# Optimization experiments

Measured on AMD Instinct MI355X. Metric: run time of the kernel, lower is better.

## Reference

```python
import jax, jax.numpy as jnp
import numpy as np

B, H, S, D = 2, 16, 2048, 64


def setup_inputs() -> dict:
    key = jax.random.key(0)
    kq, kk, kv, km = jax.random.split(key, 4)
    q = jax.random.normal(kq, (B, H, S, D), dtype=jnp.float32)
    k = jax.random.normal(kk, (B, H, S, D), dtype=jnp.float32)
    v = jax.random.normal(kv, (B, H, S, D), dtype=jnp.float32)
    # True = attend, False = masked out (padding)
    attention_mask = jax.random.randint(km, (B, S), 0, 2).astype(jnp.bool_)
    return {"q": q, "k": k, "v": v, "attention_mask": attention_mask}


def reference(q, k, v, attention_mask):
    scale = q.shape[-1] ** -0.5
    # sim: [B, H, S, S]
    sim = jnp.einsum("bhid,bhjd->bhij", q, k) * scale
    neg = jnp.finfo(sim.dtype).min
    # mask [B, S] -> [B, 1, 1, S]; keep where mask is True
    sim = jnp.where(attention_mask[:, None, None, :], sim, neg)
    attn = jax.nn.softmax(sim, axis=-1)
    out = jnp.einsum("bhij,bhjd->bhid", attn, v)
    return out
```

## Files before the change

### kernel.cpp

```cpp
#include <hip/hip_runtime.h>
#include <hip/hip_fp16.h>

namespace {
constexpr int kB = 2, kH = 16, kS = 2048, kD = 64, kBH = kB * kH;
constexpr int BQ = 128, BKV = 64;
constexpr int NQT = kS / BQ;

typedef _Float16 f16x8 __attribute__((ext_vector_type(8)));
typedef _Float16 f16x4 __attribute__((ext_vector_type(4)));
typedef __fp16 fp16x2 __attribute__((ext_vector_type(2)));
typedef float f32x16 __attribute__((ext_vector_type(16)));
typedef float f32x4 __attribute__((ext_vector_type(4)));
typedef unsigned int u32;

constexpr float kQScale = 0.125f * 1.4426950408889634f;

__device__ __forceinline__ int paddr(int row, int col) {
  const int prow = row >> 1;
  return prow * 128 + ((((row & 1) << 6) | col) ^ ((prow & 15) << 3));
}

__device__ __forceinline__ u32 pkrtz(float a, float b) {
  union { fp16x2 h; u32 u; } c;
  c.h = __builtin_amdgcn_cvt_pkrtz(a, b);
  return c.u;
}

__global__ __launch_bounds__(256) void scan_kernel(const int* __restrict__ M,
                                                   int* __restrict__ Idx,
                                                   int* __restrict__ NTarr,
                                                   int* __restrict__ Nvarr) {
  const int b = blockIdx.x;
  const int tid = threadIdx.x;
  __shared__ int part[256];
  __shared__ int nvs;
  int m[8], sum = 0;
#pragma unroll
  for (int i = 0; i < 8; ++i) {
    m[i] = M[b * kS + tid * 8 + i];
    sum += m[i] ? 1 : 0;
  }
  part[tid] = sum;
  __syncthreads();
  for (int off = 1; off < 256; off <<= 1) {
    int v = (tid >= off) ? part[tid - off] : 0;
    __syncthreads();
    part[tid] += v;
    __syncthreads();
  }
  int run = part[tid] - sum;
#pragma unroll
  for (int i = 0; i < 8; ++i)
    if (m[i]) Idx[b * kS + run++] = tid * 8 + i;
  if (tid == 255) nvs = part[255];
  __syncthreads();
  const int Nv = nvs;
  int NT = (Nv + 63) >> 6;
  if (NT == 0) NT = 1;
  const int pad = NT * 64;
  for (int j = Nv + tid; j < pad; j += 256) Idx[b * kS + j] = 0;
  if (tid == 0) { NTarr[b] = NT; Nvarr[b] = Nv; }
}

__global__ __launch_bounds__(256) void gather_kv_kernel(
    const float* __restrict__ K, const float* __restrict__ V,
    const int* __restrict__ Idx, const int* __restrict__ NTarr,
    _Float16* __restrict__ Kc, _Float16* __restrict__ Vtc) {
  __shared__ _Float16 Vl[64 * 68];
  __shared__ int ridx[64];
  const int tid = threadIdx.x;
  const int bh = blockIdx.x >> 5;
  const int jt = blockIdx.x & 31;
  const int b = bh >> 4;
  if (jt >= NTarr[b]) return;
  if (tid < 64) ridx[tid] = Idx[b * kS + jt * 64 + tid];
  __syncthreads();

  const float* kbase = K + (size_t)bh * kS * kD;
  _Float16* kout = Kc + ((size_t)bh * kS + jt * 64) * kD;
#pragma unroll
  for (int it = 0; it < 2; ++it) {
    const int e = tid + 256 * it;
    const int row = e >> 3, d0 = (e & 7) * 8;
    const float* p = kbase + (size_t)ridx[row] * kD + d0;
    float4 x = *(const float4*)p;
    float4 y = *(const float4*)(p + 4);
    f16x8 o;
    o[0] = (_Float16)x.x; o[1] = (_Float16)x.y; o[2] = (_Float16)x.z; o[3] = (_Float16)x.w;
    o[4] = (_Float16)y.x; o[5] = (_Float16)y.y; o[6] = (_Float16)y.z; o[7] = (_Float16)y.w;
    *(f16x8*)(kout + (size_t)row * kD + d0) = o;
  }

  const float* vb = V + (size_t)bh * kS * kD;
#pragma unroll
  for (int i = 0; i < 4; ++i) {
    int off = (tid + 256 * i) * 4;
    int r = off >> 6, c = off & 63;
    float4 x = *(const float4*)(vb + (size_t)ridx[r] * kD + c);
    Vl[(c + 0) * 68 + r] = (_Float16)x.x;
    Vl[(c + 1) * 68 + r] = (_Float16)x.y;
    Vl[(c + 2) * 68 + r] = (_Float16)x.z;
    Vl[(c + 3) * 68 + r] = (_Float16)x.w;
  }
  __syncthreads();
  const int d = tid >> 2, c0 = (tid & 3) * 16;
  _Float16* op = Vtc + ((size_t)bh * kD + d) * kS + jt * 64 + c0;
#pragma unroll
  for (int j = 0; j < 4; ++j)
    *(f16x4*)(op + 4 * j) = *(const f16x4*)(Vl + d * 68 + c0 + 4 * j);
}

__global__ __launch_bounds__(256, 2) void fattn_c(
    const _Float16* __restrict__ Kc, const _Float16* __restrict__ Vtc,
    const float* __restrict__ Q, const int* __restrict__ NTarr,
    const int* __restrict__ Nvarr, float* __restrict__ O) {
  __shared__ __align__(16) char smem[32768];
  _Float16* Kl = (_Float16*)smem;
  _Float16* Vl = (_Float16*)(smem + 16384);
  float* Os = (float*)smem;

  const int tid = threadIdx.x;
  const int lane = tid & 63;
  const int w = tid >> 6;
  const int q = lane & 31;
  const int h = lane >> 5;

  const int bid = blockIdx.x;
  const int cpx = gridDim.x >> 3;
  const int sbid = (bid & 7) * cpx + (bid >> 3);
  const int bh = sbid >> 4;
  const int qt = sbid & 15;
  const int q0 = qt * BQ;
  const int b = bh >> 4;
  const int NT = NTarr[b];
  const int Nv = Nvarr[b];

  f16x8 qf[4];
  {
    const float* qp = Q + ((size_t)bh * kS + q0 + w * 32 + q) * kD;
#pragma unroll
    for (int dc = 0; dc < 4; ++dc) {
      const float* p = qp + dc * 16 + h * 8;
      float4 x = *(const float4*)p;
      float4 y = *(const float4*)(p + 4);
      f16x8 a;
      a[0] = (_Float16)(x.x * kQScale); a[1] = (_Float16)(x.y * kQScale);
      a[2] = (_Float16)(x.z * kQScale); a[3] = (_Float16)(x.w * kQScale);
      a[4] = (_Float16)(y.x * kQScale); a[5] = (_Float16)(y.y * kQScale);
      a[6] = (_Float16)(y.z * kQScale); a[7] = (_Float16)(y.w * kQScale);
      qf[dc] = a;
    }
  }

  f32x16 oa[2];
#pragma unroll
  for (int i = 0; i < 16; ++i) { oa[0][i] = 0.f; oa[1][i] = 0.f; }
  f32x16 kZero;
#pragma unroll
  for (int i = 0; i < 16; ++i) kZero[i] = 0.f;
  float m_run = -30.f, l_run = 0.f;

  const _Float16* kb = Kc + (size_t)bh * kS * kD;
  const _Float16* vb = Vtc + (size_t)bh * kD * kS;

  const int sr = tid >> 2, sc = (tid & 3) * 16;
  const int a0 = paddr(sr, sc), a1 = paddr(sr, sc + 8);

  {
    f16x8 k0 = *(const f16x8*)(kb + (size_t)sr * kD + sc);
    f16x8 k1 = *(const f16x8*)(kb + (size_t)sr * kD + sc + 8);
    f16x8 v0 = *(const f16x8*)(vb + (size_t)sr * kS + sc);
    f16x8 v1 = *(const f16x8*)(vb + (size_t)sr * kS + sc + 8);
    *(f16x8*)(Kl + a0) = k0; *(f16x8*)(Kl + a1) = k1;
    *(f16x8*)(Vl + a0) = v0; *(f16x8*)(Vl + a1) = v1;
  }
  __syncthreads();

  int cur = 0;
  for (int t = 0; t < NT; ++t) {
    const int t0 = t * BKV;
    const bool pf = (t + 1 < NT);
    f16x8 nk0, nk1, nv0, nv1;
    if (pf) {
      const int n0 = t0 + BKV;
      nk0 = *(const f16x8*)(kb + (size_t)(n0 + sr) * kD + sc);
      nk1 = *(const f16x8*)(kb + (size_t)(n0 + sr) * kD + sc + 8);
      nv0 = *(const f16x8*)(vb + (size_t)sr * kS + n0 + sc);
      nv1 = *(const f16x8*)(vb + (size_t)sr * kS + n0 + sc + 8);
    }

    const _Float16* kd = Kl + cur * 4096;
    const _Float16* vd = Vl + cur * 4096;

    f32x16 s[2];
    __builtin_amdgcn_s_setprio(1);
#pragma unroll
    for (int mt = 0; mt < 2; ++mt) {
      f32x16 z = kZero;
#pragma unroll
      for (int dc = 0; dc < 4; ++dc) {
        f16x8 kf = *(const f16x8*)(kd + paddr(mt * 32 + q, dc * 16 + h * 8));
        z = __builtin_amdgcn_mfma_f32_32x32x16_f16(kf, qf[dc], z, 0, 0, 0);
      }
      s[mt] = z;
    }
    __builtin_amdgcn_s_setprio(0);

    if (t == NT - 1) {
      const int kbase = t0 + 4 * h;
#pragma unroll
      for (int mt = 0; mt < 2; ++mt)
#pragma unroll
        for (int r = 0; r < 16; ++r) {
          const int key = kbase + mt * 32 + 8 * (r >> 2) + (r & 3);
          if (key >= Nv) s[mt][r] = -1e30f;
        }
    }

    float tm[16];
#pragma unroll
    for (int i = 0; i < 16; ++i) tm[i] = fmaxf(s[0][i], s[1][i]);
#pragma unroll
    for (int st = 8; st > 0; st >>= 1)
#pragma unroll
      for (int i = 0; i < st; ++i) tm[i] = fmaxf(tm[i], tm[i + st]);
    const float mx = fmaxf(tm[0], __shfl_xor(tm[0], 32));

    if (__any(mx > m_run + 8.f)) {
      const float mnew = fmaxf(m_run, mx);
      const float corr = __builtin_amdgcn_exp2f(m_run - mnew);
      m_run = mnew;
      l_run *= corr;
#pragma unroll
      for (int mt = 0; mt < 2; ++mt)
#pragma unroll
        for (int r = 0; r < 16; ++r) oa[mt][r] *= corr;
    }
    const float negm = -m_run;

#pragma unroll
    for (int mt = 0; mt < 2; ++mt)
#pragma unroll
      for (int r = 0; r < 16; ++r)
        s[mt][r] = __builtin_amdgcn_exp2f(s[mt][r] + negm);
    float tsum[16];
#pragma unroll
    for (int i = 0; i < 16; ++i) tsum[i] = s[0][i] + s[1][i];
#pragma unroll
    for (int st = 8; st > 0; st >>= 1)
#pragma unroll
      for (int i = 0; i < st; ++i) tsum[i] += tsum[i + st];
    l_run += tsum[0] + __shfl_xor(tsum[0], 32);

    u32 pkA[2][4], pkB[2][4];
#pragma unroll
    for (int mt = 0; mt < 2; ++mt)
#pragma unroll
      for (int g = 0; g < 4; ++g) {
        pkA[mt][g] = pkrtz(s[mt][4 * g + 0], s[mt][4 * g + 1]);
        pkB[mt][g] = pkrtz(s[mt][4 * g + 2], s[mt][4 * g + 3]);
      }

    __builtin_amdgcn_s_setprio(1);
#pragma unroll
    for (int kk = 0; kk < 4; ++kk) {
      const int e = kk & 1, mt = kk >> 1;
      u32 crossA = __shfl_xor(h ? pkA[mt][2 * e] : pkA[mt][2 * e + 1], 32);
      u32 crossB = __shfl_xor(h ? pkB[mt][2 * e] : pkB[mt][2 * e + 1], 32);
      union { u32 u[4]; f16x8 v; } pb;
      pb.u[0] = h ? crossA : pkA[mt][2 * e];
      pb.u[1] = h ? crossB : pkB[mt][2 * e];
      pb.u[2] = h ? pkA[mt][2 * e + 1] : crossA;
      pb.u[3] = h ? pkB[mt][2 * e + 1] : crossB;
#pragma unroll
      for (int md = 0; md < 2; ++md) {
        f16x8 vf = *(const f16x8*)(vd + paddr(md * 32 + q, kk * 16 + h * 8));
        oa[md] = __builtin_amdgcn_mfma_f32_32x32x16_f16(vf, pb.v, oa[md], 0, 0, 0);
      }
    }
    __builtin_amdgcn_s_setprio(0);

    if (pf) {
      _Float16* kd2 = Kl + (cur ^ 1) * 4096;
      _Float16* vd2 = Vl + (cur ^ 1) * 4096;
      *(f16x8*)(kd2 + a0) = nk0; *(f16x8*)(kd2 + a1) = nk1;
      *(f16x8*)(vd2 + a0) = nv0; *(f16x8*)(vd2 + a1) = nv1;
    }
    __syncthreads();
    cur ^= 1;
  }

  const float inv = 1.f / l_run;
#pragma unroll
  for (int ph = 0; ph < 2; ++ph) {
    __syncthreads();
    if ((w >> 1) == ph) {
#pragma unroll
      for (int mt = 0; mt < 2; ++mt)
#pragma unroll
        for (int r = 0; r < 16; ++r) {
          int d = mt * 32 + (r & 3) + 8 * (r >> 2) + 4 * h;
          Os[((w & 1) * 32 + q) * 68 + d] = oa[mt][r] * inv;
        }
    }
    __syncthreads();
    {
      const int row = tid >> 2, cb = (tid & 3) * 16;
      float* op = O + ((size_t)bh * kS + q0 + ph * 64 + row) * kD + cb;
      const float* sp = Os + row * 68 + cb;
#pragma unroll
      for (int j = 0; j < 4; ++j) *(float4*)(op + 4 * j) = *(const float4*)(sp + 4 * j);
    }
  }
}

__device__ __forceinline__ int swz(int row, int colh) {
  return row * 64 + (colh ^ ((row & 7) << 3));
}

__global__ __launch_bounds__(256, 4) void fattn_fallback(
    const float* __restrict__ Q, const float* __restrict__ K,
    const float* __restrict__ V, const int* __restrict__ M,
    float* __restrict__ O) {
  __shared__ __align__(16) _Float16 Kl[64 * 64];
  __shared__ __align__(16) _Float16 Vtl[64 * 64];
  __shared__ __align__(16) _Float16 Pl[64 * 64];
  __shared__ float mbl[64];

  const int tid = threadIdx.x;
  const int lane = tid & 63;
  const int w = tid >> 6;
  const int lr = lane & 15;
  const int hg = lane >> 4;
  const int NQT1 = kS / 64;
  const int bh = blockIdx.x / NQT1;
  const int qt = blockIdx.x % NQT1;
  const int b = bh / kH;
  const int q0 = qt * 64;

  f16x8 aq[2];
  {
    const int row = q0 + w * 16 + lr;
    const float* qp = Q + ((size_t)bh * kS + row) * kD;
#pragma unroll
    for (int kf = 0; kf < 2; ++kf) {
      const float* p = qp + kf * 32 + hg * 8;
      float4 x = *(const float4*)(p);
      float4 y = *(const float4*)(p + 4);
      f16x8 a;
      a[0] = (_Float16)(x.x * 0.125f); a[1] = (_Float16)(x.y * 0.125f);
      a[2] = (_Float16)(x.z * 0.125f); a[3] = (_Float16)(x.w * 0.125f);
      a[4] = (_Float16)(y.x * 0.125f); a[5] = (_Float16)(y.y * 0.125f);
      a[6] = (_Float16)(y.z * 0.125f); a[7] = (_Float16)(y.w * 0.125f);
      aq[kf] = a;
    }
  }

  f32x4 oacc[4];
#pragma unroll
  for (int c = 0; c < 4; ++c) { oacc[c][0]=0.f; oacc[c][1]=0.f; oacc[c][2]=0.f; oacc[c][3]=0.f; }
  float m_run[4], l_run[4];
#pragma unroll
  for (int r = 0; r < 4; ++r) { m_run[r] = -1e30f; l_run[r] = 0.f; }

  const float* kb = K + (size_t)bh * kS * kD;
  const float* vb = V + (size_t)bh * kS * kD;
  const int* mbp = M + b * kS;

  for (int t0 = 0; t0 < kS; t0 += 64) {
    __syncthreads();
#pragma unroll
    for (int i = 0; i < 4; ++i) {
      const int off = (tid + 256 * i) * 4;
      const int row = off >> 6;
      const int col = off & 63;
      float4 kx = *(const float4*)(kb + (size_t)(t0 + row) * kD + col);
      f16x4 hk;
      hk[0] = (_Float16)kx.x; hk[1] = (_Float16)kx.y;
      hk[2] = (_Float16)kx.z; hk[3] = (_Float16)kx.w;
      *(f16x4*)(Kl + swz(row, col)) = hk;
      float4 vx = *(const float4*)(vb + (size_t)(t0 + row) * kD + col);
      Vtl[swz(col + 0, row)] = (_Float16)vx.x;
      Vtl[swz(col + 1, row)] = (_Float16)vx.y;
      Vtl[swz(col + 2, row)] = (_Float16)vx.z;
      Vtl[swz(col + 3, row)] = (_Float16)vx.w;
    }
    if (tid < 64) mbl[tid] = mbp[t0 + tid] ? 0.f : -1e30f;
    __syncthreads();

    f32x4 s[4];
#pragma unroll
    for (int c = 0; c < 4; ++c) {
      f32x4 z; z[0]=0.f; z[1]=0.f; z[2]=0.f; z[3]=0.f;
#pragma unroll
      for (int kf = 0; kf < 2; ++kf) {
        f16x8 bk = *(const f16x8*)(Kl + swz(c * 16 + lr, kf * 32 + hg * 8));
        z = __builtin_amdgcn_mfma_f32_16x16x32_f16(aq[kf], bk, z, 0, 0, 0);
      }
      const float mval = mbl[c * 16 + lr];
#pragma unroll
      for (int r = 0; r < 4; ++r) z[r] += mval;
      s[c] = z;
    }

    float tmax[4];
#pragma unroll
    for (int r = 0; r < 4; ++r)
      tmax[r] = fmaxf(fmaxf(s[0][r], s[1][r]), fmaxf(s[2][r], s[3][r]));
#pragma unroll
    for (int off = 1; off < 16; off <<= 1)
#pragma unroll
      for (int r = 0; r < 4; ++r) tmax[r] = fmaxf(tmax[r], __shfl_xor(tmax[r], off));

    float mnew[4], corr[4], tsum[4];
#pragma unroll
    for (int r = 0; r < 4; ++r) {
      mnew[r] = fmaxf(m_run[r], tmax[r]);
      corr[r] = __expf(m_run[r] - mnew[r]);
      m_run[r] = mnew[r];
      tsum[r] = 0.f;
    }
#pragma unroll
    for (int c = 0; c < 4; ++c)
#pragma unroll
      for (int r = 0; r < 4; ++r) {
        const float p = __expf(s[c][r] - mnew[r]);
        tsum[r] += p;
        Pl[swz(w * 16 + hg * 4 + r, c * 16 + lr)] = (_Float16)p;
      }
#pragma unroll
    for (int off = 1; off < 16; off <<= 1)
#pragma unroll
      for (int r = 0; r < 4; ++r) tsum[r] += __shfl_xor(tsum[r], off);
#pragma unroll
    for (int r = 0; r < 4; ++r) l_run[r] = l_run[r] * corr[r] + tsum[r];
#pragma unroll
    for (int c = 0; c < 4; ++c)
#pragma unroll
      for (int r = 0; r < 4; ++r) oacc[c][r] *= corr[r];

#pragma unroll
    for (int kf = 0; kf < 2; ++kf) {
      f16x8 pa = *(const f16x8*)(Pl + swz(w * 16 + lr, kf * 32 + hg * 8));
#pragma unroll
      for (int cd = 0; cd < 4; ++cd) {
        f16x8 vbf = *(const f16x8*)(Vtl + swz(cd * 16 + lr, kf * 32 + hg * 8));
        oacc[cd] = __builtin_amdgcn_mfma_f32_16x16x32_f16(pa, vbf, oacc[cd], 0, 0, 0);
      }
    }
  }

#pragma unroll
  for (int r = 0; r < 4; ++r) {
    const float inv = 1.f / l_run[r];
    const int row = q0 + w * 16 + hg * 4 + r;
    float* op = O + ((size_t)bh * kS + row) * kD;
#pragma unroll
    for (int cd = 0; cd < 4; ++cd) op[cd * 16 + lr] = oacc[cd][r] * inv;
  }
}
}

extern "C" void kernel_launch(void* const* d_in, const int* in_sizes, int n_in,
                              void* d_out, int out_size, void* d_ws, size_t ws_size,
                              hipStream_t stream) {
  (void)in_sizes; (void)n_in; (void)out_size;
  const float* q = (const float*)d_in[0];
  const float* k = (const float*)d_in[1];
  const float* v = (const float*)d_in[2];
  const int* m = (const int*)d_in[3];
  float* o = (float*)d_out;

  const size_t elems = (size_t)kBH * kS * kD;
  const size_t need = 2 * elems * sizeof(_Float16)
                    + (size_t)kB * kS * sizeof(int)
                    + 512;

  if (ws_size >= need) {
    _Float16* Kc = (_Float16*)d_ws;
    _Float16* Vtc = Kc + elems;
    int* Idx = (int*)(Vtc + elems);
    int* NTarr = Idx + (size_t)kB * kS;
    int* Nvarr = NTarr + 64;
    hipLaunchKernelGGL(scan_kernel, dim3(kB), dim3(256), 0, stream, m, Idx, NTarr, Nvarr);
    hipLaunchKernelGGL(gather_kv_kernel, dim3(kBH * (kS / 64)), dim3(256), 0, stream,
                       k, v, Idx, NTarr, Kc, Vtc);
    hipLaunchKernelGGL(fattn_c, dim3(kBH * NQT), dim3(256), 0, stream,
                       Kc, Vtc, q, NTarr, Nvarr, o);
  } else {
    hipLaunchKernelGGL(fattn_fallback, dim3(kBH * (kS / 64)), dim3(256), 0, stream,
                       q, k, v, m, o);
  }
}
```

Baseline: 52.35 us.

## Split KV range across two warp groups per block and merge softmax partials

```diff
diff --git a/kernel.cpp b/kernel.cpp
--- a/kernel.cpp
+++ b/kernel.cpp
@@ -10,7 +10,6 @@
 typedef _Float16 f16x4 __attribute__((ext_vector_type(4)));
 typedef __fp16 fp16x2 __attribute__((ext_vector_type(2)));
 typedef float f32x16 __attribute__((ext_vector_type(16)));
-typedef float f32x4 __attribute__((ext_vector_type(4)));
 typedef unsigned int u32;
 
 constexpr float kQScale = 0.125f * 1.4426950408889634f;
@@ -57,6 +56,7 @@
   const int Nv = nvs;
   int NT = (Nv + 63) >> 6;
   if (NT == 0) NT = 1;
+  NT += (NT & 1);
   const int pad = NT * 64;
   for (int j = Nv + tid; j < pad; j += 256) Idx[b * kS + j] = 0;
   if (tid == 0) { NTarr[b] = NT; Nvarr[b] = Nv; }
@@ -110,20 +110,19 @@
     *(f16x4*)(op + 4 * j) = *(const f16x4*)(Vl + d * 68 + c0 + 4 * j);
 }
 
-__global__ __launch_bounds__(256, 2) void fattn_c(
+__global__ __launch_bounds__(512, 4) void fattn8(
     const _Float16* __restrict__ Kc, const _Float16* __restrict__ Vtc,
     const float* __restrict__ Q, const int* __restrict__ NTarr,
     const int* __restrict__ Nvarr, float* __restrict__ O) {
-  __shared__ __align__(16) char smem[32768];
-  _Float16* Kl = (_Float16*)smem;
-  _Float16* Vl = (_Float16*)(smem + 16384);
-  float* Os = (float*)smem;
+  __shared__ __align__(16) char smem[66560];
 
   const int tid = threadIdx.x;
   const int lane = tid & 63;
-  const int w = tid >> 6;
   const int q = lane & 31;
   const int h = lane >> 5;
+  const int half = tid >> 8;
+  const int ptid = tid & 255;
+  const int hw = ptid >> 6;
 
   const int bid = blockIdx.x;
   const int cpx = gridDim.x >> 3;
@@ -134,10 +133,14 @@
   const int b = bh >> 4;
   const int NT = NTarr[b];
   const int Nv = Nvarr[b];
+  const int NTh = NT >> 1;
+  const int g0 = half * NTh;
+
+  _Float16* Kl = (_Float16*)(smem + half * 16384);
 
   f16x8 qf[4];
   {
-    const float* qp = Q + ((size_t)bh * kS + q0 + w * 32 + q) * kD;
+    const float* qp = Q + ((size_t)bh * kS + q0 + hw * 32 + q) * kD;
 #pragma unroll
     for (int dc = 0; dc < 4; ++dc) {
       const float* p = qp + dc * 16 + h * 8;
@@ -155,48 +158,48 @@
   f32x16 oa[2];
 #pragma unroll
   for (int i = 0; i < 16; ++i) { oa[0][i] = 0.f; oa[1][i] = 0.f; }
-  f32x16 kZero;
-#pragma unroll
-  for (int i = 0; i < 16; ++i) kZero[i] = 0.f;
   float m_run = -30.f, l_run = 0.f;
 
   const _Float16* kb = Kc + (size_t)bh * kS * kD;
   const _Float16* vb = Vtc + (size_t)bh * kD * kS;
-
-  const int sr = tid >> 2, sc = (tid & 3) * 16;
+  const _Float16* vrow0 = vb + (size_t)q * kS + h * 8;
+  const _Float16* vrow1 = vb + (size_t)(q + 32) * kS + h * 8;
+
+  const int sr = ptid >> 2, sc = (ptid & 3) * 16;
   const int a0 = paddr(sr, sc), a1 = paddr(sr, sc + 8);
 
-  {
-    f16x8 k0 = *(const f16x8*)(kb + (size_t)sr * kD + sc);
-    f16x8 k1 = *(const f16x8*)(kb + (size_t)sr * kD + sc + 8);
-    f16x8 v0 = *(const f16x8*)(vb + (size_t)sr * kS + sc);
-    f16x8 v1 = *(const f16x8*)(vb + (size_t)sr * kS + sc + 8);
-    *(f16x8*)(Kl + a0) = k0; *(f16x8*)(Kl + a1) = k1;
-    *(f16x8*)(Vl + a0) = v0; *(f16x8*)(Vl + a1) = v1;
-  }
+  f16x8 nk0, nk1, vr[8];
+
+  nk0 = *(const f16x8*)(kb + (size_t)(g0 * 64 + sr) * kD + sc);
+  nk1 = *(const f16x8*)(kb + (size_t)(g0 * 64 + sr) * kD + sc + 8);
+  *(f16x8*)(Kl + a0) = nk0;
+  *(f16x8*)(Kl + a1) = nk1;
   __syncthreads();
 
   int cur = 0;
-  for (int t = 0; t < NT; ++t) {
-    const int t0 = t * BKV;
-    const bool pf = (t + 1 < NT);
-    f16x8 nk0, nk1, nv0, nv1;
+  for (int i = 0; i < NTh; ++i) {
+    const int g = g0 + i;
+#pragma unroll
+    for (int kk = 0; kk < 4; ++kk) {
+      vr[kk] = *(const f16x8*)(vrow0 + g * 64 + kk * 16);
+      vr[4 + kk] = *(const f16x8*)(vrow1 + g * 64 + kk * 16);
+    }
+    const bool pf = (i + 1 < NTh);
     if (pf) {
-      const int n0 = t0 + BKV;
+      const int n0 = (g + 1) * 64;
       nk0 = *(const f16x8*)(kb + (size_t)(n0 + sr) * kD + sc);
       nk1 = *(const f16x8*)(kb + (size_t)(n0 + sr) * kD + sc + 8);
-      nv0 = *(const f16x8*)(vb + (size_t)sr * kS + n0 + sc);
-      nv1 = *(const f16x8*)(vb + (size_t)sr * kS + n0 + sc + 8);
     }
 
     const _Float16* kd = Kl + cur * 4096;
-    const _Float16* vd = Vl + cur * 4096;
 
     f32x16 s[2];
     __builtin_amdgcn_s_setprio(1);
 #pragma unroll
     for (int mt = 0; mt < 2; ++mt) {
-      f32x16 z = kZero;
+      f32x16 z;
+#pragma unroll
+      for (int i2 = 0; i2 < 16; ++i2) z[i2] = 0.f;
 #pragma unroll
       for (int dc = 0; dc < 4; ++dc) {
         f16x8 kf = *(const f16x8*)(kd + paddr(mt * 32 + q, dc * 16 + h * 8));
@@ -206,8 +209,8 @@
     }
     __builtin_amdgcn_s_setprio(0);
 
-    if (t == NT - 1) {
-      const int kbase = t0 + 4 * h;
+    if ((g + 1) * 64 > Nv) {
+      const int kbase = g * 64 + 4 * h;
 #pragma unroll
       for (int mt = 0; mt < 2; ++mt)
 #pragma unroll
@@ -219,11 +222,11 @@
 
     float tm[16];
 #pragma unroll
-    for (int i = 0; i < 16; ++i) tm[i] = fmaxf(s[0][i], s[1][i]);
+    for (int i2 = 0; i2 < 16; ++i2) tm[i2] = fmaxf(s[0][i2], s[1][i2]);
 #pragma unroll
     for (int st = 8; st > 0; st >>= 1)
 #pragma unroll
-      for (int i = 0; i < st; ++i) tm[i] = fmaxf(tm[i], tm[i + st]);
+      for (int i2 = 0; i2 < st; ++i2) tm[i2] = fmaxf(tm[i2], tm[i2 + st]);
     const float mx = fmaxf(tm[0], __shfl_xor(tm[0], 32));
 
     if (__any(mx > m_run + 8.f)) {
@@ -245,20 +248,20 @@
         s[mt][r] = __builtin_amdgcn_exp2f(s[mt][r] + negm);
     float tsum[16];
 #pragma unroll
-    for (int i = 0; i < 16; ++i) tsum[i] = s[0][i] + s[1][i];
+    for (int i2 = 0; i2 < 16; ++i2) tsum[i2] = s[0][i2] + s[1][i2];
 #pragma unroll
     for (int st = 8; st > 0; st >>= 1)
 #pragma unroll
-      for (int i = 0; i < st; ++i) tsum[i] += tsum[i + st];
+      for (int i2 = 0; i2 < st; ++i2) tsum[i2] += tsum[i2 + st];
     l_run += tsum[0] + __shfl_xor(tsum[0], 32);
 
     u32 pkA[2][4], pkB[2][4];
 #pragma unroll
     for (int mt = 0; mt < 2; ++mt)
 #pragma unroll
-      for (int g = 0; g < 4; ++g) {
-        pkA[mt][g] = pkrtz(s[mt][4 * g + 0], s[mt][4 * g + 1]);
-        pkB[mt][g] = pkrtz(s[mt][4 * g + 2], s[mt][4 * g + 3]);
+      for (int g2 = 0; g2 < 4; ++g2) {
+        pkA[mt][g2] = pkrtz(s[mt][4 * g2 + 0], s[mt][4 * g2 + 1]);
+        pkB[mt][g2] = pkrtz(s[mt][4 * g2 + 2], s[mt][4 * g2 + 3]);
       }
 
     __builtin_amdgcn_s_setprio(1);
@@ -273,43 +276,66 @@
       pb.u[2] = h ? pkA[mt][2 * e + 1] : crossA;
       pb.u[3] = h ? pkB[mt][2 * e + 1] : crossB;
 #pragma unroll
-      for (int md = 0; md < 2; ++md) {
-        f16x8 vf = *(const f16x8*)(vd + paddr(md * 32 + q, kk * 16 + h * 8));
-        oa[md] = __builtin_amdgcn_mfma_f32_32x32x16_f16(vf, pb.v, oa[md], 0, 0, 0);
-      }
+      for (int md = 0; md < 2; ++md)
+        oa[md] = __builtin_amdgcn_mfma_f32_32x32x16_f16(vr[md * 4 + kk], pb.v,
+                                                        oa[md], 0, 0, 0);
     }
     __builtin_amdgcn_s_setprio(0);
 
     if (pf) {
       _Float16* kd2 = Kl + (cur ^ 1) * 4096;
-      _Float16* vd2 = Vl + (cur ^ 1) * 4096;
-      *(f16x8*)(kd2 + a0) = nk0; *(f16x8*)(kd2 + a1) = nk1;
-      *(f16x8*)(vd2 + a0) = nv0; *(f16x8*)(vd2 + a1) = nv1;
+      *(f16x8*)(kd2 + a0) = nk0;
+      *(f16x8*)(kd2 + a1) = nk1;
     }
     __syncthreads();
     cur ^= 1;
   }
 
-  const float inv = 1.f / l_run;
+  float* O1 = (float*)(smem + 32768);
+  float* ml1 = (float*)(smem + 65536);
+  if (half == 1) {
+#pragma unroll
+    for (int mt = 0; mt < 2; ++mt)
+#pragma unroll
+      for (int r = 0; r < 16; ++r) {
+        const int d = mt * 32 + (r & 3) + 8 * (r >> 2) + 4 * h;
+        O1[(hw * 32 + q) * 64 + d] = oa[mt][r];
+      }
+    if (h == 0)
+      ((float2*)ml1)[hw * 32 + q] = make_float2(m_run, l_run);
+  }
+  __syncthreads();
+  float w0 = 0.f, w1 = 0.f;
+  if (half == 0) {
+    const float2 m1 = ((const float2*)ml1)[hw * 32 + q];
+    const float mm = fmaxf(m_run, m1.x);
+    w0 = __builtin_amdgcn_exp2f(m_run - mm);
+    w1 = __builtin_amdgcn_exp2f(m1.x - mm);
+    const float inv = 1.f / (l_run * w0 + m1.y * w1);
+    w0 *= inv;
+    w1 *= inv;
+  }
+  float* Os = (float*)smem;
 #pragma unroll
   for (int ph = 0; ph < 2; ++ph) {
     __syncthreads();
-    if ((w >> 1) == ph) {
+    if (half == 0 && (hw >> 1) == ph) {
 #pragma unroll
       for (int mt = 0; mt < 2; ++mt)
 #pragma unroll
         for (int r = 0; r < 16; ++r) {
-          int d = mt * 32 + (r & 3) + 8 * (r >> 2) + 4 * h;
-          Os[((w & 1) * 32 + q) * 68 + d] = oa[mt][r] * inv;
+          const int d = mt * 32 + (r & 3) + 8 * (r >> 2) + 4 * h;
+          const int gqr = hw * 32 + q;
+          Os[((hw & 1) * 32 + q) * 68 + d] = oa[mt][r] * w0 + O1[gqr * 64 + d] * w1;
         }
     }
     __syncthreads();
     {
-      const int row = tid >> 2, cb = (tid & 3) * 16;
-      float* op = O + ((size_t)bh * kS + q0 + ph * 64 + row) * kD + cb;
-      const float* sp = Os + row * 68 + cb;
-#pragma unroll
-      for (int j = 0; j < 4; ++j) *(float4*)(op + 4 * j) = *(const float4*)(sp + 4 * j);
+      const int row = tid >> 3, c0 = (tid & 7) * 8;
+      float* op = O + ((size_t)bh * kS + q0 + ph * 64 + row) * kD + c0;
+      const float* sp = Os + row * 68 + c0;
+      *(float4*)op = *(const float4*)sp;
+      *(float4*)(op + 4) = *(const float4*)(sp + 4);
     }
   }
 }
@@ -356,6 +382,7 @@
     }
   }
 
+  typedef float f32x4 __attribute__((ext_vector_type(4)));
   f32x4 oacc[4];
 #pragma unroll
   for (int c = 0; c < 4; ++c) { oacc[c][0]=0.f; oacc[c][1]=0.f; oacc[c][2]=0.f; oacc[c][3]=0.f; }
@@ -485,7 +512,7 @@
     hipLaunchKernelGGL(scan_kernel, dim3(kB), dim3(256), 0, stream, m, Idx, NTarr, Nvarr);
     hipLaunchKernelGGL(gather_kv_kernel, dim3(kBH * (kS / 64)), dim3(256), 0, stream,
                        k, v, Idx, NTarr, Kc, Vtc);
-    hipLaunchKernelGGL(fattn_c, dim3(kBH * NQT), dim3(256), 0, stream,
+    hipLaunchKernelGGL(fattn8, dim3(kBH * NQT), dim3(512), 0, stream,
                        Kc, Vtc, q, NTarr, Nvarr, o);
   } else {
     hipLaunchKernelGGL(fattn_fallback, dim3(kBH * (kS / 64)), dim3(256), 0, stream,
```

Measured after the change: 103.5 us. +97.8%, slower.

## Process two KV tiles per iteration with 64KB double-buffered shared memory

Applied to the files above, without the earlier changes.

```diff
diff --git a/kernel.cpp b/kernel.cpp
--- a/kernel.cpp
+++ b/kernel.cpp
@@ -3,14 +3,13 @@
 
 namespace {
 constexpr int kB = 2, kH = 16, kS = 2048, kD = 64, kBH = kB * kH;
-constexpr int BQ = 128, BKV = 64;
+constexpr int BQ = 128;
 constexpr int NQT = kS / BQ;
 
 typedef _Float16 f16x8 __attribute__((ext_vector_type(8)));
 typedef _Float16 f16x4 __attribute__((ext_vector_type(4)));
 typedef __fp16 fp16x2 __attribute__((ext_vector_type(2)));
 typedef float f32x16 __attribute__((ext_vector_type(16)));
-typedef float f32x4 __attribute__((ext_vector_type(4)));
 typedef unsigned int u32;
 
 constexpr float kQScale = 0.125f * 1.4426950408889634f;
@@ -57,6 +56,7 @@
   const int Nv = nvs;
   int NT = (Nv + 63) >> 6;
   if (NT == 0) NT = 1;
+  NT += (NT & 1);
   const int pad = NT * 64;
   for (int j = Nv + tid; j < pad; j += 256) Idx[b * kS + j] = 0;
   if (tid == 0) { NTarr[b] = NT; Nvarr[b] = Nv; }
@@ -114,9 +114,9 @@
     const _Float16* __restrict__ Kc, const _Float16* __restrict__ Vtc,
     const float* __restrict__ Q, const int* __restrict__ NTarr,
     const int* __restrict__ Nvarr, float* __restrict__ O) {
-  __shared__ __align__(16) char smem[32768];
+  __shared__ __align__(16) char smem[65536];
   _Float16* Kl = (_Float16*)smem;
-  _Float16* Vl = (_Float16*)(smem + 16384);
+  _Float16* Vl = (_Float16*)(smem + 32768);
   float* Os = (float*)smem;
 
   const int tid = threadIdx.x;
@@ -134,6 +134,7 @@
   const int b = bh >> 4;
   const int NT = NTarr[b];
   const int Nv = Nvarr[b];
+  const int NP = NT >> 1;
 
   f16x8 qf[4];
   {
@@ -155,9 +156,6 @@
   f32x16 oa[2];
 #pragma unroll
   for (int i = 0; i < 16; ++i) { oa[0][i] = 0.f; oa[1][i] = 0.f; }
-  f32x16 kZero;
-#pragma unroll
-  for (int i = 0; i < 16; ++i) kZero[i] = 0.f;
   float m_run = -30.f, l_run = 0.f;
 
   const _Float16* kb = Kc + (size_t)bh * kS * kD;
@@ -166,64 +164,78 @@
   const int sr = tid >> 2, sc = (tid & 3) * 16;
   const int a0 = paddr(sr, sc), a1 = paddr(sr, sc + 8);
 
-  {
-    f16x8 k0 = *(const f16x8*)(kb + (size_t)sr * kD + sc);
-    f16x8 k1 = *(const f16x8*)(kb + (size_t)sr * kD + sc + 8);
-    f16x8 v0 = *(const f16x8*)(vb + (size_t)sr * kS + sc);
-    f16x8 v1 = *(const f16x8*)(vb + (size_t)sr * kS + sc + 8);
-    *(f16x8*)(Kl + a0) = k0; *(f16x8*)(Kl + a1) = k1;
-    *(f16x8*)(Vl + a0) = v0; *(f16x8*)(Vl + a1) = v1;
-  }
+  f16x8 nk0, nk1, nv0, nv1;
+  auto loadT = [&](int g) {
+    const _Float16* kp = kb + (size_t)(g * 64 + sr) * kD + sc;
+    const _Float16* vp = vb + (size_t)sr * kS + g * 64 + sc;
+    nk0 = *(const f16x8*)(kp);
+    nk1 = *(const f16x8*)(kp + 8);
+    nv0 = *(const f16x8*)(vp);
+    nv1 = *(const f16x8*)(vp + 8);
+  };
+  auto writeT = [&](int buf, int sub) {
+    _Float16* kd = Kl + buf * 8192 + sub * 4096;
+    _Float16* vd = Vl + buf * 8192 + sub * 4096;
+    *(f16x8*)(kd + a0) = nk0; *(f16x8*)(kd + a1) = nk1;
+    *(f16x8*)(vd + a0) = nv0; *(f16x8*)(vd + a1) = nv1;
+  };
+
+  loadT(0); writeT(0, 0);
+  loadT(1); writeT(0, 1);
   __syncthreads();
 
   int cur = 0;
-  for (int t = 0; t < NT; ++t) {
-    const int t0 = t * BKV;
-    const bool pf = (t + 1 < NT);
-    f16x8 nk0, nk1, nv0, nv1;
-    if (pf) {
-      const int n0 = t0 + BKV;
-      nk0 = *(const f16x8*)(kb + (size_t)(n0 + sr) * kD + sc);
-      nk1 = *(const f16x8*)(kb + (size_t)(n0 + sr) * kD + sc + 8);
-      nv0 = *(const f16x8*)(vb + (size_t)sr * kS + n0 + sc);
-      nv1 = *(const f16x8*)(vb + (size_t)sr * kS + n0 + sc + 8);
-    }
-
-    const _Float16* kd = Kl + cur * 4096;
-    const _Float16* vd = Vl + cur * 4096;
-
-    f32x16 s[2];
+  for (int i = 0; i < NP; ++i) {
+    const bool pf = (i + 1 < NP);
+    if (pf) loadT(2 * i + 2);
+
+    const _Float16* kd = Kl + cur * 8192;
+    const _Float16* vd = Vl + cur * 8192;
+
+    f32x16 s[4];
     __builtin_amdgcn_s_setprio(1);
 #pragma unroll
-    for (int mt = 0; mt < 2; ++mt) {
-      f32x16 z = kZero;
-#pragma unroll
-      for (int dc = 0; dc < 4; ++dc) {
-        f16x8 kf = *(const f16x8*)(kd + paddr(mt * 32 + q, dc * 16 + h * 8));
-        z = __builtin_amdgcn_mfma_f32_32x32x16_f16(kf, qf[dc], z, 0, 0, 0);
-      }
-      s[mt] = z;
-    }
+    for (int sub = 0; sub < 2; ++sub)
+#pragma unroll
+      for (int mt = 0; mt < 2; ++mt) {
+        f32x16 z;
+#pragma unroll
+        for (int i2 = 0; i2 < 16; ++i2) z[i2] = 0.f;
+#pragma unroll
+        for (int dc = 0; dc < 4; ++dc) {
+          f16x8 kf = *(const f16x8*)(kd + sub * 4096 +
+                                     paddr(mt * 32 + q, dc * 16 + h * 8));
+          z = __builtin_amdgcn_mfma_f32_32x32x16_f16(kf, qf[dc], z, 0, 0, 0);
+        }
+        s[sub * 2 + mt] = z;
+      }
     __builtin_amdgcn_s_setprio(0);
 
-    if (t == NT - 1) {
-      const int kbase = t0 + 4 * h;
-#pragma unroll
-      for (int mt = 0; mt < 2; ++mt)
-#pragma unroll
-        for (int r = 0; r < 16; ++r) {
-          const int key = kbase + mt * 32 + 8 * (r >> 2) + (r & 3);
-          if (key >= Nv) s[mt][r] = -1e30f;
-        }
+    if (pf) writeT(cur ^ 1, 0);
+    if (pf) loadT(2 * i + 3);
+
+    if ((i + 1) * 128 > Nv) {
+#pragma unroll
+      for (int sub = 0; sub < 2; ++sub) {
+        const int kbase = i * 128 + sub * 64 + 4 * h;
+#pragma unroll
+        for (int mt = 0; mt < 2; ++mt)
+#pragma unroll
+          for (int r = 0; r < 16; ++r) {
+            const int key = kbase + mt * 32 + 8 * (r >> 2) + (r & 3);
+            if (key >= Nv) s[sub * 2 + mt][r] = -1e30f;
+          }
+      }
     }
 
     float tm[16];
 #pragma unroll
-    for (int i = 0; i < 16; ++i) tm[i] = fmaxf(s[0][i], s[1][i]);
+    for (int i2 = 0; i2 < 16; ++i2)
+      tm[i2] = fmaxf(fmaxf(s[0][i2], s[1][i2]), fmaxf(s[2][i2], s[3][i2]));
 #pragma unroll
     for (int st = 8; st > 0; st >>= 1)
 #pragma unroll
-      for (int i = 0; i < st; ++i) tm[i] = fmaxf(tm[i], tm[i + st]);
+      for (int i2 = 0; i2 < st; ++i2) tm[i2] = fmaxf(tm[i2], tm[i2 + st]);
     const float mx = fmaxf(tm[0], __shfl_xor(tm[0], 32));
 
     if (__any(mx > m_run + 8.f)) {
@@ -239,53 +251,52 @@
     const float negm = -m_run;
 
 #pragma unroll
-    for (int mt = 0; mt < 2; ++mt)
+    for (int st4 = 0; st4 < 4; ++st4)
 #pragma unroll
       for (int r = 0; r < 16; ++r)
-        s[mt][r] = __builtin_amdgcn_exp2f(s[mt][r] + negm);
+        s[st4][r] = __builtin_amdgcn_exp2f(s[st4][r] + negm);
     float tsum[16];
 #pragma unroll
-    for (int i = 0; i < 16; ++i) tsum[i] = s[0][i] + s[1][i];
+    for (int i2 = 0; i2 < 16; ++i2)
+      tsum[i2] = (s[0][i2] + s[1][i2]) + (s[2][i2] + s[3][i2]);
 #pragma unroll
     for (int st = 8; st > 0; st >>= 1)
 #pragma unroll
-      for (int i = 0; i < st; ++i) tsum[i] += tsum[i + st];
+      for (int i2 = 0; i2 < st; ++i2) tsum[i2] += tsum[i2 + st];
     l_run += tsum[0] + __shfl_xor(tsum[0], 32);
 
-    u32 pkA[2][4], pkB[2][4];
-#pragma unroll
-    for (int mt = 0; mt < 2; ++mt)
-#pragma unroll
-      for (int g = 0; g < 4; ++g) {
-        pkA[mt][g] = pkrtz(s[mt][4 * g + 0], s[mt][4 * g + 1]);
-        pkB[mt][g] = pkrtz(s[mt][4 * g + 2], s[mt][4 * g + 3]);
+    u32 pkA[4][4], pkB[4][4];
+#pragma unroll
+    for (int st4 = 0; st4 < 4; ++st4)
+#pragma unroll
+      for (int g2 = 0; g2 < 4; ++g2) {
+        pkA[st4][g2] = pkrtz(s[st4][4 * g2 + 0], s[st4][4 * g2 + 1]);
+        pkB[st4][g2] = pkrtz(s[st4][4 * g2 + 2], s[st4][4 * g2 + 3]);
       }
 
     __builtin_amdgcn_s_setprio(1);
 #pragma unroll
-    for (int kk = 0; kk < 4; ++kk) {
+    for (int vkk = 0; vkk < 8; ++vkk) {
+      const int sub = vkk >> 2, kk = vkk & 3;
       const int e = kk & 1, mt = kk >> 1;
-      u32 crossA = __shfl_xor(h ? pkA[mt][2 * e] : pkA[mt][2 * e + 1], 32);
-      u32 crossB = __shfl_xor(h ? pkB[mt][2 * e] : pkB[mt][2 * e + 1], 32);
+      const int st4 = sub * 2 + mt;
+      u32 crossA = __shfl_xor(h ? pkA[st4][2 * e] : pkA[st4][2 * e + 1], 32);
+      u32 crossB = __shfl_xor(h ? pkB[st4][2 * e] : pkB[st4][2 * e + 1], 32);
       union { u32 u[4]; f16x8 v; } pb;
-      pb.u[0] = h ? crossA : pkA[mt][2 * e];
-      pb.u[1] = h ? crossB : pkB[mt][2 * e];
-      pb.u[2] = h ? pkA[mt][2 * e + 1] : crossA;
-      pb.u[3] = h ? pkB[mt][2 * e + 1] : crossB;
+      pb.u[0] = h ? crossA : pkA[st4][2 * e];
+      pb.u[1] = h ? crossB : pkB[st4][2 * e];
+      pb.u[2] = h ? pkA[st4][2 * e + 1] : crossA;
+      pb.u[3] = h ? pkB[st4][2 * e + 1] : crossB;
 #pragma unroll
       for (int md = 0; md < 2; ++md) {
-        f16x8 vf = *(const f16x8*)(vd + paddr(md * 32 + q, kk * 16 + h * 8));
+        f16x8 vf = *(const f16x8*)(vd + sub * 4096 +
+                                   paddr(md * 32 + q, kk * 16 + h * 8));
         oa[md] = __builtin_amdgcn_mfma_f32_32x32x16_f16(vf, pb.v, oa[md], 0, 0, 0);
       }
     }
     __builtin_amdgcn_s_setprio(0);
 
-    if (pf) {
-      _Float16* kd2 = Kl + (cur ^ 1) * 4096;
-      _Float16* vd2 = Vl + (cur ^ 1) * 4096;
-      *(f16x8*)(kd2 + a0) = nk0; *(f16x8*)(kd2 + a1) = nk1;
-      *(f16x8*)(vd2 + a0) = nv0; *(f16x8*)(vd2 + a1) = nv1;
-    }
+    if (pf) writeT(cur ^ 1, 1);
     __syncthreads();
     cur ^= 1;
   }
@@ -356,6 +367,7 @@
     }
   }
 
+  typedef float f32x4 __attribute__((ext_vector_type(4)));
   f32x4 oacc[4];
 #pragma unroll
   for (int c = 0; c < 4; ++c) { oacc[c][0]=0.f; oacc[c][1]=0.f; oacc[c][2]=0.f; oacc[c][3]=0.f; }
```

Result: no change. 52.03 us (-0.6%).

## Switch attention kernel to 16x16x32 MFMA with 64-row query tiles

Applied to the files above, without the earlier changes.

```diff
diff --git a/kernel.cpp b/kernel.cpp
--- a/kernel.cpp
+++ b/kernel.cpp
@@ -3,13 +3,12 @@
 
 namespace {
 constexpr int kB = 2, kH = 16, kS = 2048, kD = 64, kBH = kB * kH;
-constexpr int BQ = 128, BKV = 64;
+constexpr int BQ = 64;
 constexpr int NQT = kS / BQ;
 
 typedef _Float16 f16x8 __attribute__((ext_vector_type(8)));
 typedef _Float16 f16x4 __attribute__((ext_vector_type(4)));
 typedef __fp16 fp16x2 __attribute__((ext_vector_type(2)));
-typedef float f32x16 __attribute__((ext_vector_type(16)));
 typedef float f32x4 __attribute__((ext_vector_type(4)));
 typedef unsigned int u32;
 
@@ -110,7 +109,7 @@
     *(f16x4*)(op + 4 * j) = *(const f16x4*)(Vl + d * 68 + c0 + 4 * j);
 }
 
-__global__ __launch_bounds__(256, 2) void fattn_c(
+__global__ __launch_bounds__(256, 4) void fattn16(
     const _Float16* __restrict__ Kc, const _Float16* __restrict__ Vtc,
     const float* __restrict__ Q, const int* __restrict__ NTarr,
     const int* __restrict__ Nvarr, float* __restrict__ O) {
@@ -122,27 +121,26 @@
   const int tid = threadIdx.x;
   const int lane = tid & 63;
   const int w = tid >> 6;
-  const int q = lane & 31;
-  const int h = lane >> 5;
+  const int ql = lane & 15;
+  const int u = lane >> 4;
 
   const int bid = blockIdx.x;
   const int cpx = gridDim.x >> 3;
   const int sbid = (bid & 7) * cpx + (bid >> 3);
-  const int bh = sbid >> 4;
-  const int qt = sbid & 15;
+  const int bh = sbid >> 5;
+  const int qt = sbid & 31;
   const int q0 = qt * BQ;
   const int b = bh >> 4;
   const int NT = NTarr[b];
   const int Nv = Nvarr[b];
 
-  f16x8 qf[4];
+  f16x8 qf[2];
   {
-    const float* qp = Q + ((size_t)bh * kS + q0 + w * 32 + q) * kD;
-#pragma unroll
-    for (int dc = 0; dc < 4; ++dc) {
-      const float* p = qp + dc * 16 + h * 8;
-      float4 x = *(const float4*)p;
-      float4 y = *(const float4*)(p + 4);
+    const float* qp = Q + ((size_t)bh * kS + q0 + w * 16 + ql) * kD + u * 8;
+#pragma unroll
+    for (int dc = 0; dc < 2; ++dc) {
+      float4 x = *(const float4*)(qp + dc * 32);
+      float4 y = *(const float4*)(qp + dc * 32 + 4);
       f16x8 a;
       a[0] = (_Float16)(x.x * kQScale); a[1] = (_Float16)(x.y * kQScale);
       a[2] = (_Float16)(x.z * kQScale); a[3] = (_Float16)(x.w * kQScale);
@@ -152,12 +150,9 @@
     }
   }
 
-  f32x16 oa[2];
-#pragma unroll
-  for (int i = 0; i < 16; ++i) { oa[0][i] = 0.f; oa[1][i] = 0.f; }
-  f32x16 kZero;
-#pragma unroll
-  for (int i = 0; i < 16; ++i) kZero[i] = 0.f;
+  f32x4 oa[4];
+#pragma unroll
+  for (int dg = 0; dg < 4; ++dg) { oa[dg][0]=0.f; oa[dg][1]=0.f; oa[dg][2]=0.f; oa[dg][3]=0.f; }
   float m_run = -30.f, l_run = 0.f;
 
   const _Float16* kb = Kc + (size_t)bh * kS * kD;
@@ -166,65 +161,69 @@
   const int sr = tid >> 2, sc = (tid & 3) * 16;
   const int a0 = paddr(sr, sc), a1 = paddr(sr, sc + 8);
 
-  {
-    f16x8 k0 = *(const f16x8*)(kb + (size_t)sr * kD + sc);
-    f16x8 k1 = *(const f16x8*)(kb + (size_t)sr * kD + sc + 8);
-    f16x8 v0 = *(const f16x8*)(vb + (size_t)sr * kS + sc);
-    f16x8 v1 = *(const f16x8*)(vb + (size_t)sr * kS + sc + 8);
-    *(f16x8*)(Kl + a0) = k0; *(f16x8*)(Kl + a1) = k1;
-    *(f16x8*)(Vl + a0) = v0; *(f16x8*)(Vl + a1) = v1;
-  }
-  __syncthreads();
+  f16x8 nk0, nk1, nv0, nv1;
+  auto loadT = [&](int g) {
+    const _Float16* kp = kb + (size_t)(g * 64 + sr) * kD + sc;
+    const _Float16* vp = vb + (size_t)sr * kS + g * 64 + sc;
+    nk0 = *(const f16x8*)(kp);
+    nk1 = *(const f16x8*)(kp + 8);
+    nv0 = *(const f16x8*)(vp);
+    nv1 = *(const f16x8*)(vp + 8);
+  };
+  auto writeT = [&](int buf) {
+    _Float16* kd = Kl + buf * 4096;
+    _Float16* vd = Vl + buf * 4096;
+    *(f16x8*)(kd + a0) = nk0; *(f16x8*)(kd + a1) = nk1;
+    *(f16x8*)(vd + a0) = nv0; *(f16x8*)(vd + a1) = nv1;
+  };
+
+  loadT(0);
+  writeT(0);
+  __syncthreads();
+
+  const int src1 = ql + ((u & 1) << 5);
 
   int cur = 0;
   for (int t = 0; t < NT; ++t) {
-    const int t0 = t * BKV;
     const bool pf = (t + 1 < NT);
-    f16x8 nk0, nk1, nv0, nv1;
-    if (pf) {
-      const int n0 = t0 + BKV;
-      nk0 = *(const f16x8*)(kb + (size_t)(n0 + sr) * kD + sc);
-      nk1 = *(const f16x8*)(kb + (size_t)(n0 + sr) * kD + sc + 8);
-      nv0 = *(const f16x8*)(vb + (size_t)sr * kS + n0 + sc);
-      nv1 = *(const f16x8*)(vb + (size_t)sr * kS + n0 + sc + 8);
-    }
+    if (pf) loadT(t + 1);
 
     const _Float16* kd = Kl + cur * 4096;
     const _Float16* vd = Vl + cur * 4096;
 
-    f32x16 s[2];
+    f32x4 s[4];
     __builtin_amdgcn_s_setprio(1);
 #pragma unroll
-    for (int mt = 0; mt < 2; ++mt) {
-      f32x16 z = kZero;
-#pragma unroll
-      for (int dc = 0; dc < 4; ++dc) {
-        f16x8 kf = *(const f16x8*)(kd + paddr(mt * 32 + q, dc * 16 + h * 8));
-        z = __builtin_amdgcn_mfma_f32_32x32x16_f16(kf, qf[dc], z, 0, 0, 0);
-      }
-      s[mt] = z;
+    for (int kg = 0; kg < 4; ++kg) {
+      f32x4 z; z[0]=0.f; z[1]=0.f; z[2]=0.f; z[3]=0.f;
+#pragma unroll
+      for (int dc = 0; dc < 2; ++dc) {
+        f16x8 kf = *(const f16x8*)(kd + paddr(kg * 16 + ql, dc * 32 + u * 8));
+        z = __builtin_amdgcn_mfma_f32_16x16x32_f16(kf, qf[dc], z, 0, 0, 0);
+      }
+      s[kg] = z;
     }
     __builtin_amdgcn_s_setprio(0);
 
-    if (t == NT - 1) {
-      const int kbase = t0 + 4 * h;
-#pragma unroll
-      for (int mt = 0; mt < 2; ++mt)
-#pragma unroll
-        for (int r = 0; r < 16; ++r) {
-          const int key = kbase + mt * 32 + 8 * (r >> 2) + (r & 3);
-          if (key >= Nv) s[mt][r] = -1e30f;
-        }
-    }
-
-    float tm[16];
-#pragma unroll
-    for (int i = 0; i < 16; ++i) tm[i] = fmaxf(s[0][i], s[1][i]);
-#pragma unroll
-    for (int st = 8; st > 0; st >>= 1)
+    if ((t + 1) * 64 > Nv) {
+      const int kb0 = t * 64 + u * 4;
+#pragma unroll
+      for (int kg = 0; kg < 4; ++kg)
+#pragma unroll
+        for (int j = 0; j < 4; ++j)
+          if (kb0 + kg * 16 + j >= Nv) s[kg][j] = -1e30f;
+    }
+
+    float tm[8];
+#pragma unroll
+    for (int i = 0; i < 8; ++i) tm[i] = fmaxf(s[i >> 2][i & 3], s[2 + (i >> 2)][i & 3]);
+#pragma unroll
+    for (int st = 4; st > 0; st >>= 1)
 #pragma unroll
       for (int i = 0; i < st; ++i) tm[i] = fmaxf(tm[i], tm[i + st]);
-    const float mx = fmaxf(tm[0], __shfl_xor(tm[0], 32));
+    float mx = tm[0];
+    mx = fmaxf(mx, __shfl_xor(mx, 16));
+    mx = fmaxf(mx, __shfl_xor(mx, 32));
 
     if (__any(mx > m_run + 8.f)) {
       const float mnew = fmaxf(m_run, mx);
@@ -232,85 +231,75 @@
       m_run = mnew;
       l_run *= corr;
 #pragma unroll
-      for (int mt = 0; mt < 2; ++mt)
-#pragma unroll
-        for (int r = 0; r < 16; ++r) oa[mt][r] *= corr;
+      for (int dg = 0; dg < 4; ++dg)
+#pragma unroll
+        for (int j = 0; j < 4; ++j) oa[dg][j] *= corr;
     }
     const float negm = -m_run;
 
 #pragma unroll
-    for (int mt = 0; mt < 2; ++mt)
-#pragma unroll
-      for (int r = 0; r < 16; ++r)
-        s[mt][r] = __builtin_amdgcn_exp2f(s[mt][r] + negm);
-    float tsum[16];
-#pragma unroll
-    for (int i = 0; i < 16; ++i) tsum[i] = s[0][i] + s[1][i];
-#pragma unroll
-    for (int st = 8; st > 0; st >>= 1)
+    for (int kg = 0; kg < 4; ++kg)
+#pragma unroll
+      for (int j = 0; j < 4; ++j)
+        s[kg][j] = __builtin_amdgcn_exp2f(s[kg][j] + negm);
+    float tsum[8];
+#pragma unroll
+    for (int i = 0; i < 8; ++i) tsum[i] = s[i >> 2][i & 3] + s[2 + (i >> 2)][i & 3];
+#pragma unroll
+    for (int st = 4; st > 0; st >>= 1)
 #pragma unroll
       for (int i = 0; i < st; ++i) tsum[i] += tsum[i + st];
-    l_run += tsum[0] + __shfl_xor(tsum[0], 32);
-
-    u32 pkA[2][4], pkB[2][4];
-#pragma unroll
-    for (int mt = 0; mt < 2; ++mt)
-#pragma unroll
-      for (int g = 0; g < 4; ++g) {
-        pkA[mt][g] = pkrtz(s[mt][4 * g + 0], s[mt][4 * g + 1]);
-        pkB[mt][g] = pkrtz(s[mt][4 * g + 2], s[mt][4 * g + 3]);
-      }
+    float ts = tsum[0];
+    ts += __shfl_xor(ts, 16);
+    ts += __shfl_xor(ts, 32);
+    l_run += ts;
+
+    u32 pkA[4], pkB[4];
+#pragma unroll
+    for (int kg = 0; kg < 4; ++kg) {
+      pkA[kg] = pkrtz(s[kg][0], s[kg][1]);
+      pkB[kg] = pkrtz(s[kg][2], s[kg][3]);
+    }
 
     __builtin_amdgcn_s_setprio(1);
 #pragma unroll
-    for (int kk = 0; kk < 4; ++kk) {
-      const int e = kk & 1, mt = kk >> 1;
-      u32 crossA = __shfl_xor(h ? pkA[mt][2 * e] : pkA[mt][2 * e + 1], 32);
-      u32 crossB = __shfl_xor(h ? pkB[mt][2 * e] : pkB[mt][2 * e + 1], 32);
-      union { u32 u[4]; f16x8 v; } pb;
-      pb.u[0] = h ? crossA : pkA[mt][2 * e];
-      pb.u[1] = h ? crossB : pkB[mt][2 * e];
-      pb.u[2] = h ? pkA[mt][2 * e + 1] : crossA;
-      pb.u[3] = h ? pkB[mt][2 * e + 1] : crossB;
-#pragma unroll
-      for (int md = 0; md < 2; ++md) {
-        f16x8 vf = *(const f16x8*)(vd + paddr(md * 32 + q, kk * 16 + h * 8));
-        oa[md] = __builtin_amdgcn_mfma_f32_32x32x16_f16(vf, pb.v, oa[md], 0, 0, 0);
+    for (int kc = 0; kc < 2; ++kc) {
+      union { u32 uu[4]; f16x8 v; } pb;
+#pragma unroll
+      for (int hb = 0; hb < 2; ++hb) {
+        const int kgn = (kc << 1) | hb;
+        u32 a1 = (u32)__shfl((int)pkA[kgn], src1);
+        u32 b1 = (u32)__shfl((int)pkB[kgn], src1);
+        u32 a2 = (u32)__shfl((int)pkA[kgn], src1 + 16);
+        u32 b2 = (u32)__shfl((int)pkB[kgn], src1 + 16);
+        if ((u >> 1) == hb) { pb.uu[0] = a1; pb.uu[1] = b1; pb.uu[2] = a2; pb.uu[3] = b2; }
+      }
+#pragma unroll
+      for (int dg = 0; dg < 4; ++dg) {
+        f16x8 vf = *(const f16x8*)(vd + paddr(dg * 16 + ql, kc * 32 + u * 8));
+        oa[dg] = __builtin_amdgcn_mfma_f32_16x16x32_f16(vf, pb.v, oa[dg], 0, 0, 0);
       }
     }
     __builtin_amdgcn_s_setprio(0);
 
-    if (pf) {
-      _Float16* kd2 = Kl + (cur ^ 1) * 4096;
-      _Float16* vd2 = Vl + (cur ^ 1) * 4096;
-      *(f16x8*)(kd2 + a0) = nk0; *(f16x8*)(kd2 + a1) = nk1;
-      *(f16x8*)(vd2 + a0) = nv0; *(f16x8*)(vd2 + a1) = nv1;
-    }
+    if (pf) writeT(cur ^ 1);
     __syncthreads();
     cur ^= 1;
   }
 
   const float inv = 1.f / l_run;
 #pragma unroll
-  for (int ph = 0; ph < 2; ++ph) {
-    __syncthreads();
-    if ((w >> 1) == ph) {
-#pragma unroll
-      for (int mt = 0; mt < 2; ++mt)
-#pragma unroll
-        for (int r = 0; r < 16; ++r) {
-          int d = mt * 32 + (r & 3) + 8 * (r >> 2) + 4 * h;
-          Os[((w & 1) * 32 + q) * 68 + d] = oa[mt][r] * inv;
-        }
-    }
-    __syncthreads();
-    {
-      const int row = tid >> 2, cb = (tid & 3) * 16;
-      float* op = O + ((size_t)bh * kS + q0 + ph * 64 + row) * kD + cb;
-      const float* sp = Os + row * 68 + cb;
-#pragma unroll
-      for (int j = 0; j < 4; ++j) *(float4*)(op + 4 * j) = *(const float4*)(sp + 4 * j);
-    }
+  for (int dg = 0; dg < 4; ++dg)
+#pragma unroll
+    for (int j = 0; j < 4; ++j)
+      Os[(w * 16 + ql) * 68 + dg * 16 + u * 4 + j] = oa[dg][j] * inv;
+  __syncthreads();
+  {
+    const int row = tid >> 2, cb = (tid & 3) * 16;
+    float* op = O + ((size_t)bh * kS + q0 + row) * kD + cb;
+    const float* sp = Os + row * 68 + cb;
+#pragma unroll
+    for (int j = 0; j < 4; ++j) *(float4*)(op + 4 * j) = *(const float4*)(sp + 4 * j);
   }
 }
 
@@ -485,7 +474,7 @@
     hipLaunchKernelGGL(scan_kernel, dim3(kB), dim3(256), 0, stream, m, Idx, NTarr, Nvarr);
     hipLaunchKernelGGL(gather_kv_kernel, dim3(kBH * (kS / 64)), dim3(256), 0, stream,
                        k, v, Idx, NTarr, Kc, Vtc);
-    hipLaunchKernelGGL(fattn_c, dim3(kBH * NQT), dim3(256), 0, stream,
+    hipLaunchKernelGGL(fattn16, dim3(kBH * NQT), dim3(256), 0, stream,
                        Kc, Vtc, q, NTarr, Nvarr, o);
   } else {
     hipLaunchKernelGGL(fattn_fallback, dim3(kBH * (kS / 64)), dim3(256), 0, stream,
```

Measured after the change: 58.99 us. 1.13x slower.
